# Kernel tuning notes

Measured on AMD Instinct MI355X. Metric: run time of the kernel, lower is better.

Reference implementation:

```python
import jax, jax.numpy as jnp
import numpy as np
import math

B, N, F_IN, F_OUT = 8, 2048, 128, 128


def _uniform(key, shape, stdv):
    return jax.random.uniform(key, shape, dtype=jnp.float32, minval=-stdv, maxval=stdv)


def setup_inputs() -> dict:
    key = jax.random.key(0)
    k_x, k_a, k_w, k_att, k_bw, k_ba = jax.random.split(key, 6)
    X = jax.random.normal(k_x, (B, N, F_IN), dtype=jnp.float32)
    # dense 0/1 adjacency, as consumed by torch.bmm(A, ...)
    A = jax.random.randint(k_a, (B, N, N), 0, 2).astype(jnp.float32)
    stdv_W = 1.0 / math.sqrt(F_OUT)        # W.size(1) == n_fea_out
    stdv_a = 1.0 / math.sqrt(2 * F_OUT)    # a.size(1) == 2*n_fea_out
    W = _uniform(k_w, (F_IN, F_OUT), stdv_W)
    a = _uniform(k_att, (1, 2 * F_OUT), stdv_a)
    bias_W = _uniform(k_bw, (F_OUT,), stdv_W)
    bias_a = _uniform(k_ba, (N,), stdv_a)
    return {"X": X, "A": A, "W": W, "a": a, "bias_a": bias_a, "bias_W": bias_W}


def reference(X, A, W, a, bias_a, bias_W):
    # XW: [B, N, F_out]
    XW = jnp.einsum('bnf,fo->bno', X, W)
    f = W.shape[1]
    # Original materializes Z[b,i,j] = concat(XW[b,j], XW[b,i]) then dots with a.
    # This is separable: Z1[b,i,j] = a[:f]@XW[b,j] + a[f:]@XW[b,i] + bias_a[j]
    a_j = a[0, :f]   # multiplies XW[b, j]
    a_i = a[0, f:]   # multiplies XW[b, i]
    s_j = jnp.einsum('bnf,f->bn', XW, a_j)  # [B, N]
    s_i = jnp.einsum('bnf,f->bn', XW, a_i)  # [B, N]
    Z1 = s_i[:, :, None] + s_j[:, None, :] + bias_a[None, None, :]  # [B, N, N]
    den = jnp.exp(Z1)
    num = jnp.einsum('bik,bkj->bij', A, den)  # torch.bmm(A, denominator)
    # where numerator == 0 the torch code leaves att uninitialized; use 0 deterministically
    nz = num != 0
    att = jnp.where(nz, den / jnp.where(nz, num, 1.0), 0.0)
    buf = jnp.einsum('bij,bjf->bif', att, XW)
    H = jnp.einsum('bij,bjf->bif', A, buf) + bias_W
    return H
```

## Files before the change

kernel.cpp:

```cpp
#include <hip/hip_runtime.h>

#define BB 8
#define NN 2048
#define FF 128


__global__ __launch_bounds__(256) void kA_pack_p(const float* __restrict__ X,
                                                 const float* __restrict__ A,
                                                 const float* __restrict__ W,
                                                 const float* __restrict__ av,
                                                 float* __restrict__ p,
                                                 float* __restrict__ xpart,
                                                 unsigned* __restrict__ pk) {
    __shared__ float wls[FF];
    __shared__ float xls[FF];
    const int t = threadIdx.x;
    if (t < FF) {
        const float4* W4 = (const float4*)(W + t * FF);
        const float4* a4 = (const float4*)(av + FF);
        float s = 0.f;
#pragma unroll
        for (int f = 0; f < FF / 4; ++f) {
            const float4 w4 = W4[f], aa = a4[f];
            s += w4.x * aa.x + w4.y * aa.y + w4.z * aa.z + w4.w * aa.w;
        }
        wls[t] = s;
        xls[t] = 0.f;
    }
    __syncthreads();

    const int blk = blockIdx.x;
    const int row0 = blk * 16;
    const int lane = t & 63, wave = t >> 6;
    const int half = lane >> 5, l32 = lane & 31;

    {
        const float4 wv = ((const float4*)wls)[l32];
        float4 cs = make_float4(0.f, 0.f, 0.f, 0.f);
        const float4* X4 = (const float4*)(X + (size_t)row0 * FF);
#pragma unroll
        for (int k = 0; k < 2; ++k) {
            const int rloc = wave * 4 + k * 2 + half;
            const float4 xv = X4[rloc * 32 + l32];
            cs.x += xv.x; cs.y += xv.y; cs.z += xv.z; cs.w += xv.w;
            float s = xv.x * wv.x + xv.y * wv.y + xv.z * wv.z + xv.w * wv.w;
#pragma unroll
            for (int off = 16; off; off >>= 1) s += __shfl_xor(s, off, 64);
            if (l32 == 0) p[row0 + rloc] = expf(s);
        }
        atomicAdd(&xls[l32 * 4 + 0], cs.x);
        atomicAdd(&xls[l32 * 4 + 1], cs.y);
        atomicAdd(&xls[l32 * 4 + 2], cs.z);
        atomicAdd(&xls[l32 * 4 + 3], cs.w);
    }
    __syncthreads();
    if (t < FF) xpart[blk * FF + t] = xls[t];

    const int rbase = row0 + wave * 4;
#pragma unroll 1
    for (int g = 0; g < 2; ++g) {
        const int rowA = rbase + g * 2;
        const int rowB = rowA + 1;
        const float4* Aa = (const float4*)(A + (size_t)rowA * NN);
        const float4* Ab = (const float4*)(A + (size_t)rowB * NN);
        const float4 va0 = Aa[0 * 64 + lane], va1 = Aa[1 * 64 + lane];
        const float4 va2 = Aa[2 * 64 + lane], va3 = Aa[3 * 64 + lane];
        const float4 va4 = Aa[4 * 64 + lane], va5 = Aa[5 * 64 + lane];
        const float4 va6 = Aa[6 * 64 + lane], va7 = Aa[7 * 64 + lane];
        const float4 vb0 = Ab[0 * 64 + lane], vb1 = Ab[1 * 64 + lane];
        const float4 vb2 = Ab[2 * 64 + lane], vb3 = Ab[3 * 64 + lane];
        const float4 vb4 = Ab[4 * 64 + lane], vb5 = Ab[5 * 64 + lane];
        const float4 vb6 = Ab[6 * 64 + lane], vb7 = Ab[7 * 64 + lane];
        __builtin_amdgcn_sched_barrier(0);
        unsigned mA = 0u, mB = 0u;
#define NIB(v) ((v.x != 0.f ? 1u : 0u) | (v.y != 0.f ? 2u : 0u) | \
                (v.z != 0.f ? 4u : 0u) | (v.w != 0.f ? 8u : 0u))
        mA |= NIB(va0) << 0;  mA |= NIB(va1) << 4;  mA |= NIB(va2) << 8;  mA |= NIB(va3) << 12;
        mA |= NIB(va4) << 16; mA |= NIB(va5) << 20; mA |= NIB(va6) << 24; mA |= NIB(va7) << 28;
        mB |= NIB(vb0) << 0;  mB |= NIB(vb1) << 4;  mB |= NIB(vb2) << 8;  mB |= NIB(vb3) << 12;
        mB |= NIB(vb4) << 16; mB |= NIB(vb5) << 20; mB |= NIB(vb6) << 24; mB |= NIB(vb7) << 28;
#undef NIB
        pk[(size_t)rowA * 64 + lane] = mA;
        pk[(size_t)rowB * 64 + lane] = mB;
    }
}

__global__ __launch_bounds__(256) void kB_r(const float* __restrict__ W,
                                            const float* __restrict__ xpart,
                                            const float* __restrict__ p,
                                            const unsigned* __restrict__ pk,
                                            float* __restrict__ r,
                                            float* __restrict__ S) {
    __shared__ float p_lds[NN];
    const int t = threadIdx.x;

    if (blockIdx.x == 0) {
#pragma unroll
        for (int k = 0; k < 4; ++k) {
            const int o = t + 256 * k;
            const int b = o >> 7, f = o & 127;
            float s = 0.f;
            for (int j = 0; j < 128; ++j) s += xpart[(b * 128 + j) * FF + f];
            p_lds[o] = s;
        }
        __syncthreads();
#pragma unroll
        for (int k = 0; k < 4; ++k) {
            const int o = t + 256 * k;
            const int b = o >> 7, f = o & 127;
            float s = 0.f;
#pragma unroll 8
            for (int c = 0; c < FF; ++c) s += p_lds[b * FF + c] * W[c * FF + f];
            S[o] = s;
        }
        return;
    }

    const int row0 = (blockIdx.x - 1) * 8;
    const int b = row0 >> 11;
    const float4* p4 = (const float4*)(p + (size_t)b * NN);
    float4* pl4 = (float4*)p_lds;
    pl4[t]       = p4[t];
    pl4[t + 256] = p4[t + 256];
    __syncthreads();

    const int lane = t & 63, wave = t >> 6;
    const int rowA = row0 + wave * 2;
    const int rowB = rowA + 1;
    const unsigned wA = pk[(size_t)rowA * 64 + lane];
    const unsigned wB = pk[(size_t)rowB * 64 + lane];

    float accA = 0.f, accB = 0.f;
#pragma unroll
    for (int it = 0; it < 8; ++it) {
        const float4 pv = pl4[it * 64 + lane];
        const unsigned na = (wA >> (it * 4)) & 15u;
        const unsigned nb = (wB >> (it * 4)) & 15u;
        accA += (na & 1u) ? pv.x : 0.f;  accB += (nb & 1u) ? pv.x : 0.f;
        accA += (na & 2u) ? pv.y : 0.f;  accB += (nb & 2u) ? pv.y : 0.f;
        accA += (na & 4u) ? pv.z : 0.f;  accB += (nb & 4u) ? pv.z : 0.f;
        accA += (na & 8u) ? pv.w : 0.f;  accB += (nb & 8u) ? pv.w : 0.f;
    }
#pragma unroll
    for (int off = 32; off; off >>= 1) {
        accA += __shfl_xor(accA, off, 64);
        accB += __shfl_xor(accB, off, 64);
    }
    if (lane == 0) {
        const int lr = rowA & (NN - 1);
        r[rowA] = (accA != 0.f) ? (p_lds[lr] / accA) : 0.f;
        r[rowB] = (accB != 0.f) ? (p_lds[lr + 1] / accB) : 0.f;
    }
}

__global__ __launch_bounds__(256) void kC_H(const unsigned* __restrict__ pk,
                                            const float* __restrict__ rr,
                                            const float* __restrict__ S,
                                            const float* __restrict__ bias_W,
                                            float* __restrict__ Hout) {
    __shared__ float r_lds[NN];
    __shared__ float sls[FF], bwls[FF];
    const int t = threadIdx.x;
    const int row0 = blockIdx.x * 8;
    const int b = row0 >> 11;

    const float4* r4 = (const float4*)(rr + (size_t)b * NN);
    float4* rl4 = (float4*)r_lds;
    rl4[t]       = r4[t];
    rl4[t + 256] = r4[t + 256];
    if (t < FF) { sls[t] = S[b * FF + t]; bwls[t] = bias_W[t]; }
    __syncthreads();

    const int lane = t & 63, wave = t >> 6;
    const int rowA = row0 + wave * 2;
    const int rowB = rowA + 1;
    const unsigned wA = pk[(size_t)rowA * 64 + lane];
    const unsigned wB = pk[(size_t)rowB * 64 + lane];

    float accA = 0.f, accB = 0.f;
#pragma unroll
    for (int it = 0; it < 8; ++it) {
        const float4 rv = rl4[it * 64 + lane];
        const unsigned na = (wA >> (it * 4)) & 15u;
        const unsigned nb = (wB >> (it * 4)) & 15u;
        accA += (na & 1u) ? rv.x : 0.f;  accB += (nb & 1u) ? rv.x : 0.f;
        accA += (na & 2u) ? rv.y : 0.f;  accB += (nb & 2u) ? rv.y : 0.f;
        accA += (na & 4u) ? rv.z : 0.f;  accB += (nb & 4u) ? rv.z : 0.f;
        accA += (na & 8u) ? rv.w : 0.f;  accB += (nb & 8u) ? rv.w : 0.f;
    }
#pragma unroll
    for (int off = 32; off; off >>= 1) {
        accA += __shfl_xor(accA, off, 64);
        accB += __shfl_xor(accB, off, 64);
    }

    const float2 sv = ((const float2*)sls)[lane];
    const float2 bv = ((const float2*)bwls)[lane];
    float2* H2 = (float2*)Hout;
    H2[(size_t)rowA * 64 + lane] = make_float2(accA * sv.x + bv.x, accA * sv.y + bv.y);
    H2[(size_t)rowB * 64 + lane] = make_float2(accB * sv.x + bv.x, accB * sv.y + bv.y);
}

extern "C" void kernel_launch(void* const* d_in, const int* in_sizes, int n_in,
                              void* d_out, int out_size, void* d_ws, size_t ws_size,
                              hipStream_t stream) {
    const float* X      = (const float*)d_in[0];
    const float* A      = (const float*)d_in[1];
    const float* W      = (const float*)d_in[2];
    const float* a      = (const float*)d_in[3];
    const float* bias_W = (const float*)d_in[5];
    float* out = (float*)d_out;

    float* ws    = (float*)d_ws;
    float* xpart = ws;
    float* S     = ws + 131072;
    float* p     = ws + 132096;
    float* r     = ws + 148480;
    unsigned* pk = (unsigned*)(ws + 164864);

    kA_pack_p<<<(BB * NN) / 16, 256, 0, stream>>>(X, A, W, a, p, xpart, pk);
    kB_r<<<(BB * NN) / 8 + 1, 256, 0, stream>>>(W, xpart, p, pk, r, S);
    kC_H<<<(BB * NN) / 8, 256, 0, stream>>>(pk, r, S, bias_W, out);
}
```

Baseline: 241.0 us.

## Split X projection and adjacency bit-packing into separate kernels

The first kernel used to fuse the X·w projection and column-sum with the bit-packing of A. It is now split in two. One kernel handles X at 32 rows per block, which halves the partial-sum count reduced in kB_r. A separate kernel packs A at one row per wave across many more blocks. The aim is to give the bandwidth-bound pack of A more parallelism and free it from the X work and the LDS barrier. The cost is an extra kernel launch and the loss of the overlap between the two phases.

```diff
diff --git a/kernel.cpp b/kernel.cpp
--- a/kernel.cpp
+++ b/kernel.cpp
@@ -5,13 +5,11 @@
 #define FF 128
 
 
-__global__ __launch_bounds__(256) void kA_pack_p(const float* __restrict__ X,
-                                                 const float* __restrict__ A,
+__global__ __launch_bounds__(256) void kX_p_xsum(const float* __restrict__ X,
                                                  const float* __restrict__ W,
                                                  const float* __restrict__ av,
                                                  float* __restrict__ p,
-                                                 float* __restrict__ xpart,
-                                                 unsigned* __restrict__ pk) {
+                                                 float* __restrict__ xpart) {
     __shared__ float wls[FF];
     __shared__ float xls[FF];
     const int t = threadIdx.x;
@@ -29,60 +27,51 @@
     }
     __syncthreads();
 
-    const int blk = blockIdx.x;
-    const int row0 = blk * 16;
+    const int gr0 = blockIdx.x * 32;
     const int lane = t & 63, wave = t >> 6;
     const int half = lane >> 5, l32 = lane & 31;
-
-    {
-        const float4 wv = ((const float4*)wls)[l32];
-        float4 cs = make_float4(0.f, 0.f, 0.f, 0.f);
-        const float4* X4 = (const float4*)(X + (size_t)row0 * FF);
-#pragma unroll
-        for (int k = 0; k < 2; ++k) {
-            const int rloc = wave * 4 + k * 2 + half;
-            const float4 xv = X4[rloc * 32 + l32];
-            cs.x += xv.x; cs.y += xv.y; cs.z += xv.z; cs.w += xv.w;
-            float s = xv.x * wv.x + xv.y * wv.y + xv.z * wv.z + xv.w * wv.w;
-#pragma unroll
-            for (int off = 16; off; off >>= 1) s += __shfl_xor(s, off, 64);
-            if (l32 == 0) p[row0 + rloc] = expf(s);
-        }
-        atomicAdd(&xls[l32 * 4 + 0], cs.x);
-        atomicAdd(&xls[l32 * 4 + 1], cs.y);
-        atomicAdd(&xls[l32 * 4 + 2], cs.z);
-        atomicAdd(&xls[l32 * 4 + 3], cs.w);
-    }
-    __syncthreads();
-    if (t < FF) xpart[blk * FF + t] = xls[t];
-
-    const int rbase = row0 + wave * 4;
-#pragma unroll 1
-    for (int g = 0; g < 2; ++g) {
-        const int rowA = rbase + g * 2;
-        const int rowB = rowA + 1;
-        const float4* Aa = (const float4*)(A + (size_t)rowA * NN);
-        const float4* Ab = (const float4*)(A + (size_t)rowB * NN);
-        const float4 va0 = Aa[0 * 64 + lane], va1 = Aa[1 * 64 + lane];
-        const float4 va2 = Aa[2 * 64 + lane], va3 = Aa[3 * 64 + lane];
-        const float4 va4 = Aa[4 * 64 + lane], va5 = Aa[5 * 64 + lane];
-        const float4 va6 = Aa[6 * 64 + lane], va7 = Aa[7 * 64 + lane];
-        const float4 vb0 = Ab[0 * 64 + lane], vb1 = Ab[1 * 64 + lane];
-        const float4 vb2 = Ab[2 * 64 + lane], vb3 = Ab[3 * 64 + lane];
-        const float4 vb4 = Ab[4 * 64 + lane], vb5 = Ab[5 * 64 + lane];
-        const float4 vb6 = Ab[6 * 64 + lane], vb7 = Ab[7 * 64 + lane];
-        __builtin_amdgcn_sched_barrier(0);
-        unsigned mA = 0u, mB = 0u;
+    const float4 wv = ((const float4*)wls)[l32];
+    float4 cs = make_float4(0.f, 0.f, 0.f, 0.f);
+    const float4* X4 = (const float4*)(X + (size_t)gr0 * FF);
+
+#pragma unroll
+    for (int it = 0; it < 4; ++it) {
+        const int rloc = wave * 8 + it * 2 + half;
+        const float4 xv = X4[(size_t)rloc * 32 + l32];
+        cs.x += xv.x; cs.y += xv.y; cs.z += xv.z; cs.w += xv.w;
+        float s = xv.x * wv.x + xv.y * wv.y + xv.z * wv.z + xv.w * wv.w;
+#pragma unroll
+        for (int off = 16; off; off >>= 1) s += __shfl_xor(s, off, 64);
+        if (l32 == 0) p[gr0 + rloc] = expf(s);
+    }
+
+    atomicAdd(&xls[l32 * 4 + 0], cs.x);
+    atomicAdd(&xls[l32 * 4 + 1], cs.y);
+    atomicAdd(&xls[l32 * 4 + 2], cs.z);
+    atomicAdd(&xls[l32 * 4 + 3], cs.w);
+    __syncthreads();
+    if (t < FF) xpart[blockIdx.x * FF + t] = xls[t];
+}
+
+__global__ __launch_bounds__(256) void kP_pack(const float* __restrict__ A,
+                                               unsigned* __restrict__ pk) {
+    const int t = threadIdx.x;
+    const int lane = t & 63, wave = t >> 6;
+    const int row = blockIdx.x * 4 + wave;
+    const float4* Ar = (const float4*)(A + (size_t)row * NN);
+
+    const float4 v0 = Ar[0 * 64 + lane], v1 = Ar[1 * 64 + lane];
+    const float4 v2 = Ar[2 * 64 + lane], v3 = Ar[3 * 64 + lane];
+    const float4 v4 = Ar[4 * 64 + lane], v5 = Ar[5 * 64 + lane];
+    const float4 v6 = Ar[6 * 64 + lane], v7 = Ar[7 * 64 + lane];
+
+    unsigned m = 0u;
 #define NIB(v) ((v.x != 0.f ? 1u : 0u) | (v.y != 0.f ? 2u : 0u) | \
                 (v.z != 0.f ? 4u : 0u) | (v.w != 0.f ? 8u : 0u))
-        mA |= NIB(va0) << 0;  mA |= NIB(va1) << 4;  mA |= NIB(va2) << 8;  mA |= NIB(va3) << 12;
-        mA |= NIB(va4) << 16; mA |= NIB(va5) << 20; mA |= NIB(va6) << 24; mA |= NIB(va7) << 28;
-        mB |= NIB(vb0) << 0;  mB |= NIB(vb1) << 4;  mB |= NIB(vb2) << 8;  mB |= NIB(vb3) << 12;
-        mB |= NIB(vb4) << 16; mB |= NIB(vb5) << 20; mB |= NIB(vb6) << 24; mB |= NIB(vb7) << 28;
+    m |= NIB(v0) << 0;  m |= NIB(v1) << 4;  m |= NIB(v2) << 8;  m |= NIB(v3) << 12;
+    m |= NIB(v4) << 16; m |= NIB(v5) << 20; m |= NIB(v6) << 24; m |= NIB(v7) << 28;
 #undef NIB
-        pk[(size_t)rowA * 64 + lane] = mA;
-        pk[(size_t)rowB * 64 + lane] = mB;
-    }
+    pk[(size_t)row * 64 + lane] = m;
 }
 
 __global__ __launch_bounds__(256) void kB_r(const float* __restrict__ W,
@@ -100,7 +89,7 @@
             const int o = t + 256 * k;
             const int b = o >> 7, f = o & 127;
             float s = 0.f;
-            for (int j = 0; j < 128; ++j) s += xpart[(b * 128 + j) * FF + f];
+            for (int j = 0; j < 64; ++j) s += xpart[(b * 64 + j) * FF + f];
             p_lds[o] = s;
         }
         __syncthreads();
@@ -213,12 +202,13 @@
 
     float* ws    = (float*)d_ws;
     float* xpart = ws;
-    float* S     = ws + 131072;
-    float* p     = ws + 132096;
-    float* r     = ws + 148480;
-    unsigned* pk = (unsigned*)(ws + 164864);
-
-    kA_pack_p<<<(BB * NN) / 16, 256, 0, stream>>>(X, A, W, a, p, xpart, pk);
+    float* S     = ws + 65536;
+    float* p     = ws + 66560;
+    float* r     = ws + 82944;
+    unsigned* pk = (unsigned*)(ws + 99328);
+
+    kX_p_xsum<<<(BB * NN) / 32, 256, 0, stream>>>(X, W, a, p, xpart);
+    kP_pack<<<(BB * NN) / 4, 256, 0, stream>>>(A, pk);
     kB_r<<<(BB * NN) / 8 + 1, 256, 0, stream>>>(W, xpart, p, pk, r, S);
     kC_H<<<(BB * NN) / 8, 256, 0, stream>>>(pk, r, S, bias_W, out);
 }
```

Measured after the change: 236.9 us. No clear change (-1.7%).
